# Kernel tuning notes

Hardware: AMD Instinct MI355X
Metric: run time of the kernel (lower is better)

## Reference

```python
import jax, jax.numpy as jnp
import numpy as np

NUM_SLOTS = 128
HIDDEN_DIM = 4096
EMA_ALPHA = 0.1
WRITE_TOP_K = 2048
T_TOKENS = 8192
K_RET = 4
BATCH_IDX = 0


def setup_inputs() -> dict:
    key = jax.random.key(0)
    k1, k2, k3, k4, k5 = jax.random.split(key, 5)
    hidden_states = jax.random.normal(k1, (T_TOKENS, HIDDEN_DIM), dtype=jnp.float32)
    # attention weights over K retrieved slots: normalized to a distribution per token
    raw = jax.random.uniform(k2, (T_TOKENS, K_RET), dtype=jnp.float32)
    attention_weights = raw / raw.sum(axis=-1, keepdims=True)
    slot_indices = jax.random.randint(k3, (T_TOKENS, K_RET), 0, NUM_SLOTS)
    memory = jax.random.normal(k4, (1, NUM_SLOTS, HIDDEN_DIM), dtype=jnp.float32)
    W_imp = jax.random.normal(k5, (1, HIDDEN_DIM), dtype=jnp.float32) * 0.02
    b_imp = jnp.zeros((1,), dtype=jnp.float32)
    return {
        "hidden_states": hidden_states,
        "attention_weights": attention_weights,
        "slot_indices": slot_indices,
        "memory": memory,
        "W_imp": W_imp,
        "b_imp": b_imp,
    }


def _compute_importance(hidden_states, attention_weights, W_imp, b_imp):
    # magnitude: ||h_t||_2, [T]
    magnitude = jnp.linalg.norm(hidden_states, axis=-1)
    # attention surprise: normalized entropy over K slots, [T]
    attn = attention_weights
    entropy = -(attn * jnp.log(attn + 1e-8)).sum(axis=-1)
    max_entropy = jnp.log(jnp.asarray(attn.shape[-1], dtype=jnp.float32))
    surprise = entropy / jnp.maximum(max_entropy, 1e-8)
    importance = magnitude * (1.0 + surprise)  # 'combined' mode
    learned_score = hidden_states @ W_imp[0] + b_imp[0]  # [T]
    return importance + jax.nn.sigmoid(learned_score)


def reference(hidden_states, attention_weights, slot_indices, memory, W_imp, b_imp):
    # importance-based top-K token selection
    importance = _compute_importance(hidden_states, attention_weights, W_imp, b_imp)
    _, topk_idx = jax.lax.top_k(importance, WRITE_TOP_K)
    h_sel = hidden_states[topk_idx]          # [Ksel, D]
    si_sel = slot_indices[topk_idx]          # [Ksel, K]

    # membership[t, n] = 1 if slot n appears anywhere in token t's retrieved slots
    # (matches torch's (slot_indices == idx).any(dim=-1))
    onehot = jax.nn.one_hot(si_sel, NUM_SLOTS, dtype=jnp.float32)  # [Ksel, K, N]
    member = (onehot.sum(axis=1) > 0).astype(jnp.float32)          # [Ksel, N]

    counts = member.sum(axis=0)                                    # [N]
    sums = jnp.einsum("tn,td->nd", member, h_sel)                  # [N, D]
    agg = sums / jnp.maximum(counts, 1.0)[:, None]                 # segment mean

    current = memory[BATCH_IDX]                                    # [N, D]
    updated = EMA_ALPHA * agg + (1.0 - EMA_ALPHA) * current
    new_slots = jnp.where(counts[:, None] > 0, updated, current)
    return memory.at[BATCH_IDX].set(new_slots)
```

## Files before the change

### kernel.cpp

```cpp
#include <hip/hip_runtime.h>
#include <math.h>

#define T_TOK 8192
#define HDIM 4096
#define NSLOT 128
#define KRET 4
#define TOPK 2048
#define ALPHA 0.1f
#define MAXC 2048

__global__ __launch_bounds__(256) void importance_kernel(
    const float* __restrict__ h, const float* __restrict__ attn,
    const float* __restrict__ W, const float* __restrict__ b,
    float* __restrict__ imp, int* __restrict__ rank)
{
    const int t = blockIdx.x;
    const float4* hv = reinterpret_cast<const float4*>(h + (size_t)t * HDIM);
    const float4* Wv = reinterpret_cast<const float4*>(W);
    float sumsq = 0.f, dot = 0.f;
    for (int i = threadIdx.x; i < HDIM / 4; i += 256) {
        float4 x = hv[i];
        float4 w = Wv[i];
        sumsq += x.x * x.x + x.y * x.y + x.z * x.z + x.w * x.w;
        dot   += x.x * w.x + x.y * w.y + x.z * w.z + x.w * w.w;
    }
    #pragma unroll
    for (int off = 32; off > 0; off >>= 1) {
        sumsq += __shfl_down(sumsq, off);
        dot   += __shfl_down(dot, off);
    }
    __shared__ float s_sq[4], s_dot[4];
    const int lane = threadIdx.x & 63, wid = threadIdx.x >> 6;
    if (lane == 0) { s_sq[wid] = sumsq; s_dot[wid] = dot; }
    __syncthreads();
    if (threadIdx.x == 0) {
        float sq = s_sq[0] + s_sq[1] + s_sq[2] + s_sq[3];
        float dt = s_dot[0] + s_dot[1] + s_dot[2] + s_dot[3];
        float mag = sqrtf(sq);
        float ent = 0.f;
        #pragma unroll
        for (int k = 0; k < KRET; k++) {
            float a = attn[t * KRET + k];
            ent -= a * logf(a + 1e-8f);
        }
        float surprise = ent / logf(4.0f);
        float score = dt + b[0];
        float sig = 1.0f / (1.0f + expf(-score));
        imp[t] = mag * (1.0f + surprise) + sig;
        rank[t] = 0;
    }
}

__global__ __launch_bounds__(256) void rank_kernel(
    const float* __restrict__ imp, int* __restrict__ rank)
{
    const int cb = blockIdx.x & 31;
    const int sl = blockIdx.x >> 5;
    __shared__ float tile[256];
    const int base = sl * 256;
    tile[threadIdx.x] = imp[base + threadIdx.x];
    __syncthreads();
    const int t = cb * 256 + threadIdx.x;
    const float mine = imp[t];
    int r = 0;
    #pragma unroll 8
    for (int i = 0; i < 256; i++) {
        float v = tile[i];
        int s = base + i;
        r += (v > mine) || (v == mine && s < t);
    }
    if (r) atomicAdd(&rank[t], r);
}

__global__ __launch_bounds__(1024) void compact_kernel(
    const int* __restrict__ rank, const int* __restrict__ si,
    int* __restrict__ sel_tok, unsigned int* __restrict__ packed)
{
    __shared__ int part[1024];
    const int tid = threadIdx.x;
    const int base = tid * 8;
    int f[8];
    int local = 0;
    #pragma unroll
    for (int j = 0; j < 8; j++) {
        f[j] = (rank[base + j] < TOPK) ? 1 : 0;
        local += f[j];
    }
    part[tid] = local;
    __syncthreads();
    for (int off = 1; off < 1024; off <<= 1) {
        int v = part[tid];
        int add = (tid >= off) ? part[tid - off] : 0;
        __syncthreads();
        part[tid] = v + add;
        __syncthreads();
    }
    int pos = part[tid] - local;
    #pragma unroll
    for (int j = 0; j < 8; j++) {
        int t = base + j;
        if (f[j]) {
            int s0 = si[t * 4 + 0], s1 = si[t * 4 + 1];
            int s2 = si[t * 4 + 2], s3 = si[t * 4 + 3];
            sel_tok[pos] = t;
            packed[pos] = (unsigned)s0 | ((unsigned)s1 << 8) |
                          ((unsigned)s2 << 16) | ((unsigned)s3 << 24);
            pos++;
        }
    }
}

__global__ __launch_bounds__(256) void slotlist_kernel(
    const int* __restrict__ sel_tok, const unsigned int* __restrict__ packed,
    int* __restrict__ lists, int* __restrict__ counts)
{
    const int slot = blockIdx.x;
    const unsigned pat = (unsigned)slot * 0x01010101u;
    const int tid = threadIdx.x;
    __shared__ int part[256];
    const int base = tid * 8;
    int f[8];
    int local = 0;
    #pragma unroll
    for (int j = 0; j < 8; j++) {
        unsigned p = packed[base + j] ^ pat;
        f[j] = (((p - 0x01010101u) & ~p & 0x80808080u) != 0u) ? 1 : 0;
        local += f[j];
    }
    part[tid] = local;
    __syncthreads();
    for (int off = 1; off < 256; off <<= 1) {
        int v = part[tid];
        int add = (tid >= off) ? part[tid - off] : 0;
        __syncthreads();
        part[tid] = v + add;
        __syncthreads();
    }
    int pos = part[tid] - local;
    int* mylist = lists + (size_t)slot * MAXC;
    #pragma unroll
    for (int j = 0; j < 8; j++) {
        if (f[j]) mylist[pos++] = sel_tok[base + j];
    }
    if (tid == 255) counts[slot] = part[255];
}

__global__ __launch_bounds__(256) void update_kernel(
    const float* __restrict__ h, const float* __restrict__ mem,
    const int* __restrict__ lists, const int* __restrict__ counts,
    float* __restrict__ out)
{
    const int slot = blockIdx.x >> 2;
    const int chunk = blockIdx.x & 3;
    const int cnt = counts[slot];
    __shared__ int s_list[MAXC];
    for (int i = threadIdx.x; i < cnt; i += 256)
        s_list[i] = lists[(size_t)slot * MAXC + i];
    __syncthreads();

    const int dbase = chunk * 1024 + threadIdx.x * 4;
    float4 acc = make_float4(0.f, 0.f, 0.f, 0.f);
    int i = 0;
    for (; i + 4 <= cnt; i += 4) {
        int t0 = s_list[i], t1 = s_list[i + 1];
        int t2 = s_list[i + 2], t3 = s_list[i + 3];
        float4 x0 = *reinterpret_cast<const float4*>(h + (size_t)t0 * HDIM + dbase);
        float4 x1 = *reinterpret_cast<const float4*>(h + (size_t)t1 * HDIM + dbase);
        float4 x2 = *reinterpret_cast<const float4*>(h + (size_t)t2 * HDIM + dbase);
        float4 x3 = *reinterpret_cast<const float4*>(h + (size_t)t3 * HDIM + dbase);
        acc.x += x0.x + x1.x + x2.x + x3.x;
        acc.y += x0.y + x1.y + x2.y + x3.y;
        acc.z += x0.z + x1.z + x2.z + x3.z;
        acc.w += x0.w + x1.w + x2.w + x3.w;
    }
    for (; i < cnt; i++) {
        int t0 = s_list[i];
        float4 x0 = *reinterpret_cast<const float4*>(h + (size_t)t0 * HDIM + dbase);
        acc.x += x0.x; acc.y += x0.y; acc.z += x0.z; acc.w += x0.w;
    }

    const size_t o = (size_t)slot * HDIM + dbase;
    float4 cur = *reinterpret_cast<const float4*>(mem + o);
    float4 r;
    if (cnt > 0) {
        float inv = 1.0f / (float)cnt;
        r.x = ALPHA * (acc.x * inv) + (1.f - ALPHA) * cur.x;
        r.y = ALPHA * (acc.y * inv) + (1.f - ALPHA) * cur.y;
        r.z = ALPHA * (acc.z * inv) + (1.f - ALPHA) * cur.z;
        r.w = ALPHA * (acc.w * inv) + (1.f - ALPHA) * cur.w;
    } else {
        r = cur;
    }
    *reinterpret_cast<float4*>(out + o) = r;
}

extern "C" void kernel_launch(void* const* d_in, const int* in_sizes, int n_in,
                              void* d_out, int out_size, void* d_ws, size_t ws_size,
                              hipStream_t stream) {
    const float* h    = (const float*)d_in[0];
    const float* attn = (const float*)d_in[1];
    const int*   si   = (const int*)d_in[2];
    const float* mem  = (const float*)d_in[3];
    const float* W    = (const float*)d_in[4];
    const float* b    = (const float*)d_in[5];
    float* out = (float*)d_out;

    char* ws = (char*)d_ws;
    float*        imp     = (float*)(ws);
    int*          rank    = (int*)(ws + 32768);
    int*          sel_tok = (int*)(ws + 65536);
    unsigned int* packed  = (unsigned int*)(ws + 73728);
    int*          counts  = (int*)(ws + 81920);
    int*          lists   = (int*)(ws + 131072);

    importance_kernel<<<T_TOK, 256, 0, stream>>>(h, attn, W, b, imp, rank);
    rank_kernel<<<1024, 256, 0, stream>>>(imp, rank);
    compact_kernel<<<1, 1024, 0, stream>>>(rank, si, sel_tok, packed);
    slotlist_kernel<<<NSLOT, 256, 0, stream>>>(sel_tok, packed, lists, counts);
    update_kernel<<<NSLOT * 4, 256, 0, stream>>>(h, mem, lists, counts, out);
}
```

Measured before the change: 61.17 us.

## Merge compaction into per-slot list kernel and use one wave per token

The single-block compact kernel is removed. Each slot block now scans all 8192 tokens itself, testing the rank and the slot indices directly and writing token ids into its list. The importance kernel now maps one 64-lane wavefront to each token, with four tokens per block, so the shared-memory reduction and block barrier go away. This saves a serialized single-block launch, at the cost of every slot block reading the full rank and slot-index arrays (redundant reads that should be L2-resident).

```diff
diff --git a/kernel.cpp b/kernel.cpp
--- a/kernel.cpp
+++ b/kernel.cpp
@@ -14,13 +14,16 @@
     const float* __restrict__ W, const float* __restrict__ b,
     float* __restrict__ imp, int* __restrict__ rank)
 {
-    const int t = blockIdx.x;
+    const int wid  = threadIdx.x >> 6;
+    const int lane = threadIdx.x & 63;
+    const int t = blockIdx.x * 4 + wid;
     const float4* hv = reinterpret_cast<const float4*>(h + (size_t)t * HDIM);
     const float4* Wv = reinterpret_cast<const float4*>(W);
     float sumsq = 0.f, dot = 0.f;
-    for (int i = threadIdx.x; i < HDIM / 4; i += 256) {
-        float4 x = hv[i];
-        float4 w = Wv[i];
+    #pragma unroll 4
+    for (int i = 0; i < 16; i++) {
+        float4 x = hv[lane + i * 64];
+        float4 w = Wv[lane + i * 64];
         sumsq += x.x * x.x + x.y * x.y + x.z * x.z + x.w * x.w;
         dot   += x.x * w.x + x.y * w.y + x.z * w.z + x.w * w.w;
     }
@@ -29,14 +32,8 @@
         sumsq += __shfl_down(sumsq, off);
         dot   += __shfl_down(dot, off);
     }
-    __shared__ float s_sq[4], s_dot[4];
-    const int lane = threadIdx.x & 63, wid = threadIdx.x >> 6;
-    if (lane == 0) { s_sq[wid] = sumsq; s_dot[wid] = dot; }
-    __syncthreads();
-    if (threadIdx.x == 0) {
-        float sq = s_sq[0] + s_sq[1] + s_sq[2] + s_sq[3];
-        float dt = s_dot[0] + s_dot[1] + s_dot[2] + s_dot[3];
-        float mag = sqrtf(sq);
+    if (lane == 0) {
+        float mag = sqrtf(sumsq);
         float ent = 0.f;
         #pragma unroll
         for (int k = 0; k < KRET; k++) {
@@ -44,7 +41,7 @@
             ent -= a * logf(a + 1e-8f);
         }
         float surprise = ent / logf(4.0f);
-        float score = dt + b[0];
+        float score = dot + b[0];
         float sig = 1.0f / (1.0f + expf(-score));
         imp[t] = mag * (1.0f + surprise) + sig;
         rank[t] = 0;
@@ -72,60 +69,24 @@
     if (r) atomicAdd(&rank[t], r);
 }
 
-__global__ __launch_bounds__(1024) void compact_kernel(
+__global__ __launch_bounds__(256) void slotlist_kernel(
     const int* __restrict__ rank, const int* __restrict__ si,
-    int* __restrict__ sel_tok, unsigned int* __restrict__ packed)
-{
-    __shared__ int part[1024];
-    const int tid = threadIdx.x;
-    const int base = tid * 8;
-    int f[8];
-    int local = 0;
-    #pragma unroll
-    for (int j = 0; j < 8; j++) {
-        f[j] = (rank[base + j] < TOPK) ? 1 : 0;
-        local += f[j];
-    }
-    part[tid] = local;
-    __syncthreads();
-    for (int off = 1; off < 1024; off <<= 1) {
-        int v = part[tid];
-        int add = (tid >= off) ? part[tid - off] : 0;
-        __syncthreads();
-        part[tid] = v + add;
-        __syncthreads();
-    }
-    int pos = part[tid] - local;
-    #pragma unroll
-    for (int j = 0; j < 8; j++) {
-        int t = base + j;
-        if (f[j]) {
-            int s0 = si[t * 4 + 0], s1 = si[t * 4 + 1];
-            int s2 = si[t * 4 + 2], s3 = si[t * 4 + 3];
-            sel_tok[pos] = t;
-            packed[pos] = (unsigned)s0 | ((unsigned)s1 << 8) |
-                          ((unsigned)s2 << 16) | ((unsigned)s3 << 24);
-            pos++;
-        }
-    }
-}
-
-__global__ __launch_bounds__(256) void slotlist_kernel(
-    const int* __restrict__ sel_tok, const unsigned int* __restrict__ packed,
     int* __restrict__ lists, int* __restrict__ counts)
 {
     const int slot = blockIdx.x;
-    const unsigned pat = (unsigned)slot * 0x01010101u;
     const int tid = threadIdx.x;
     __shared__ int part[256];
-    const int base = tid * 8;
-    int f[8];
+    const int base = tid * 32;
+    unsigned mask = 0;
     int local = 0;
-    #pragma unroll
-    for (int j = 0; j < 8; j++) {
-        unsigned p = packed[base + j] ^ pat;
-        f[j] = (((p - 0x01010101u) & ~p & 0x80808080u) != 0u) ? 1 : 0;
-        local += f[j];
+    const int4* si4 = reinterpret_cast<const int4*>(si);
+    #pragma unroll 8
+    for (int j = 0; j < 32; j++) {
+        const int t = base + j;
+        int4 s = si4[t];
+        bool sel = rank[t] < TOPK;
+        bool mem = (s.x == slot) | (s.y == slot) | (s.z == slot) | (s.w == slot);
+        if (sel && mem) { mask |= (1u << j); local++; }
     }
     part[tid] = local;
     __syncthreads();
@@ -138,9 +99,8 @@
     }
     int pos = part[tid] - local;
     int* mylist = lists + (size_t)slot * MAXC;
-    #pragma unroll
-    for (int j = 0; j < 8; j++) {
-        if (f[j]) mylist[pos++] = sel_tok[base + j];
+    for (int j = 0; j < 32; j++) {
+        if (mask & (1u << j)) mylist[pos++] = base + j;
     }
     if (tid == 255) counts[slot] = part[255];
 }
@@ -206,16 +166,13 @@
     float* out = (float*)d_out;
 
     char* ws = (char*)d_ws;
-    float*        imp     = (float*)(ws);
-    int*          rank    = (int*)(ws + 32768);
-    int*          sel_tok = (int*)(ws + 65536);
-    unsigned int* packed  = (unsigned int*)(ws + 73728);
-    int*          counts  = (int*)(ws + 81920);
-    int*          lists   = (int*)(ws + 131072);
+    float* imp    = (float*)(ws);
+    int*   rank   = (int*)(ws + 32768);
+    int*   counts = (int*)(ws + 65536);
+    int*   lists  = (int*)(ws + 131072);
 
-    importance_kernel<<<T_TOK, 256, 0, stream>>>(h, attn, W, b, imp, rank);
+    importance_kernel<<<T_TOK / 4, 256, 0, stream>>>(h, attn, W, b, imp, rank);
     rank_kernel<<<1024, 256, 0, stream>>>(imp, rank);
-    compact_kernel<<<1, 1024, 0, stream>>>(rank, si, sel_tok, packed);
-    slotlist_kernel<<<NSLOT, 256, 0, stream>>>(sel_tok, packed, lists, counts);
+    slotlist_kernel<<<NSLOT, 256, 0, stream>>>(rank, si, lists, counts);
     update_kernel<<<NSLOT * 4, 256, 0, stream>>>(h, mem, lists, counts, out);
 }
```

New measurement: 59.90 us, median of 2. -2.1%, faster.
